# Performance work log

Measured on AMD Instinct MI355X. Metric: run time of the kernel, lower is better.

Reference implementation:

```python
import jax, jax.numpy as jnp
import numpy as np

C = 256      # MSA_channels
PC = 256     # pair_channels
G = 4        # groups
GP = C // G  # group_planes
FF = 4 * C
EPS = 1e-5


def layernorm(x, w, b):
    mu = jnp.mean(x, axis=-1, keepdims=True)
    var = jnp.mean(jnp.square(x - mu), axis=-1, keepdims=True)
    return (x - mu) * jax.lax.rsqrt(var + EPS) * w + b


def setup_inputs() -> dict:
    key = jax.random.key(0)
    ks = jax.random.split(key, 12)
    N, D, L = 1, 64, 512
    s = lambda fan_in: 1.0 / np.sqrt(fan_in)
    return {
        "msa_matrix": jax.random.normal(ks[0], (N, D, L, C), jnp.float32),
        "rr_edge": jax.random.normal(ks[1], (N, L, L, PC), jnp.float32),
        "ln_msa_w": jnp.ones((C,), jnp.float32),
        "ln_msa_b": jnp.zeros((C,), jnp.float32),
        "ln_rr_w": jnp.ones((PC,), jnp.float32),
        "ln_rr_b": jnp.zeros((PC,), jnp.float32),
        "WA": jax.random.normal(ks[2], (PC, G), jnp.float32) * s(PC),
        "bA": jnp.zeros((G,), jnp.float32),
        "WV": jax.random.normal(ks[3], (C, C), jnp.float32) * s(C),
        "bV": jnp.zeros((C,), jnp.float32),
        "WO": jax.random.normal(ks[4], (C, C), jnp.float32) * s(C),
        "bO": jnp.zeros((C,), jnp.float32),
        "ln_ff_w": jnp.ones((C,), jnp.float32),
        "ln_ff_b": jnp.zeros((C,), jnp.float32),
        "W1": jax.random.normal(ks[5], (C, FF), jnp.float32) * s(C),
        "b1": jnp.zeros((FF,), jnp.float32),
        "W2": jax.random.normal(ks[6], (FF, C), jnp.float32) * s(FF),
        "b2": jnp.zeros((C,), jnp.float32),
    }


def reference(msa_matrix, rr_edge, ln_msa_w, ln_msa_b, ln_rr_w, ln_rr_b,
              WA, bA, WV, bV, WO, bO, ln_ff_w, ln_ff_b, W1, b1, W2, b2):
    N, D, L, _ = msa_matrix.shape
    raw = msa_matrix
    m = layernorm(msa_matrix, ln_msa_w, ln_msa_b)          # [N,D,L,C]
    E = 0.5 * (rr_edge + jnp.swapaxes(rr_edge, 1, 2))      # symmetrize [N,L,L,PC]
    E = layernorm(E, ln_rr_w, ln_rr_b)
    A = jax.nn.softmax(E @ WA + bA, axis=2)                # [N,L,L,G], softmax over key dim j
    V = (m @ WV + bV).reshape(N, D, L, G, GP)              # [N,D,L,G,GP]
    agg = jnp.einsum('nijg,ndjgc->ndigc', A, V).reshape(N, D, L, C)
    out = agg @ WO + bO
    x = raw + out                                          # residual (dropout = identity at eval)
    h = layernorm(x, ln_ff_w, ln_ff_b)                     # FFN with pre-LN + residual
    return x + (jax.nn.relu(h @ W1 + b1) @ W2 + b2)
```

## Files before the change

### kernel.cpp

```cpp
#include <hip/hip_runtime.h>
#include <hip/hip_bf16.h>

typedef __bf16 bf16;
typedef bf16 bf16x8 __attribute__((ext_vector_type(8)));
typedef bf16 bf16x4v __attribute__((ext_vector_type(4)));
typedef float f32x4 __attribute__((ext_vector_type(4)));

#define LN_EPS 1e-5f

__global__ __launch_bounds__(256) void ln_rows_kernel(
    const float* __restrict__ in, const float* __restrict__ w,
    const float* __restrict__ b, bf16* __restrict__ out)
{
  int row = blockIdx.x * 4 + (threadIdx.x >> 6);
  int lane = threadIdx.x & 63;
  const float4* p = (const float4*)(in + (size_t)row * 256);
  float4 v = p[lane];
  float s = v.x + v.y + v.z + v.w;
  float q = v.x*v.x + v.y*v.y + v.z*v.z + v.w*v.w;
  #pragma unroll
  for (int o = 32; o; o >>= 1) { s += __shfl_xor(s, o); q += __shfl_xor(q, o); }
  float mu = s * (1.0f/256.0f);
  float rs = rsqrtf(q*(1.0f/256.0f) - mu*mu + LN_EPS);
  float4 wv = ((const float4*)w)[lane];
  float4 bv = ((const float4*)b)[lane];
  bf16x4v o4;
  o4[0] = (bf16)((v.x - mu)*rs*wv.x + bv.x);
  o4[1] = (bf16)((v.y - mu)*rs*wv.y + bv.y);
  o4[2] = (bf16)((v.z - mu)*rs*wv.z + bv.z);
  o4[3] = (bf16)((v.w - mu)*rs*wv.w + bv.w);
  *(bf16x4v*)(out + (size_t)row * 256 + lane * 4) = o4;
}

__global__ __launch_bounds__(256) void transpose_f32_bf16(
    const float* __restrict__ in, bf16* __restrict__ out, int R, int C)
{
  __shared__ float tile[32][33];
  int bc = blockIdx.x * 32, br = blockIdx.y * 32;
  int tx = threadIdx.x, ty = threadIdx.y;
  #pragma unroll
  for (int i = ty; i < 32; i += 8)
    tile[i][tx] = in[(size_t)(br + i) * C + bc + tx];
  __syncthreads();
  #pragma unroll
  for (int i = ty; i < 32; i += 8)
    out[(size_t)(bc + i) * R + br + tx] = (bf16)tile[tx][i];
}

__global__ __launch_bounds__(256) void sym_ln_wa_kernel(
    const float* __restrict__ rr, const float* __restrict__ w,
    const float* __restrict__ b, const float* __restrict__ WA,
    float* __restrict__ S)
{
  int rem = blockIdx.x; int ti = 0; int len = 32;
  while (rem >= len) { rem -= len; ti++; len--; }
  int tj = ti + rem;
  int wid = threadIdx.x >> 6, lane = threadIdx.x & 63;
  int c0 = lane * 4;
  float4 wv = ((const float4*)w)[lane];
  float4 bv = ((const float4*)b)[lane];
  const float4* wa4 = (const float4*)WA;
  float4 wa0 = wa4[c0+0], wa1 = wa4[c0+1], wa2 = wa4[c0+2], wa3 = wa4[c0+3];
  int pend = blockIdx.y * 128 + 128;
  for (int p = blockIdx.y * 128 + wid; p < pend; p += 4) {
    int i = ti*16 + (p >> 4), j = tj*16 + (p & 15);
    float4 a = ((const float4*)(rr + ((size_t)i*512 + j)*256))[lane];
    float4 c = ((const float4*)(rr + ((size_t)j*512 + i)*256))[lane];
    float ex = 0.5f*(a.x + c.x), ey = 0.5f*(a.y + c.y),
          ez = 0.5f*(a.z + c.z), ew = 0.5f*(a.w + c.w);
    float s = ex+ey+ez+ew;
    float q = ex*ex+ey*ey+ez*ez+ew*ew;
    #pragma unroll
    for (int o = 32; o; o >>= 1) { s += __shfl_xor(s, o); q += __shfl_xor(q, o); }
    float mu = s*(1.f/256.f);
    float rs = rsqrtf(q*(1.f/256.f) - mu*mu + LN_EPS);
    float nx = (ex-mu)*rs*wv.x + bv.x;
    float ny = (ey-mu)*rs*wv.y + bv.y;
    float nz = (ez-mu)*rs*wv.z + bv.z;
    float nw = (ew-mu)*rs*wv.w + bv.w;
    float g0 = nx*wa0.x + ny*wa1.x + nz*wa2.x + nw*wa3.x;
    float g1 = nx*wa0.y + ny*wa1.y + nz*wa2.y + nw*wa3.y;
    float g2 = nx*wa0.z + ny*wa1.z + nz*wa2.z + nw*wa3.z;
    float g3 = nx*wa0.w + ny*wa1.w + nz*wa2.w + nw*wa3.w;
    #pragma unroll
    for (int o = 32; o; o >>= 1) {
      g0 += __shfl_xor(g0, o); g1 += __shfl_xor(g1, o);
      g2 += __shfl_xor(g2, o); g3 += __shfl_xor(g3, o);
    }
    if (lane == 0) {
      float4 r4 = make_float4(g0, g1, g2, g3);
      ((float4*)S)[(size_t)i*512 + j] = r4;
      ((float4*)S)[(size_t)j*512 + i] = r4;
    }
  }
}

__global__ __launch_bounds__(256) void softmax_kernel(
    const float* __restrict__ S, bf16* __restrict__ Aout)
{
  int i = blockIdx.x * 4 + (threadIdx.x >> 6);
  int lane = threadIdx.x & 63;
  const float4* Sr = (const float4*)S + (size_t)i * 512;
  float4 s[8];
  float m0 = -1e30f, m1 = -1e30f, m2 = -1e30f, m3 = -1e30f;
  #pragma unroll
  for (int it = 0; it < 8; it++) {
    s[it] = Sr[lane + it*64];
    m0 = fmaxf(m0, s[it].x); m1 = fmaxf(m1, s[it].y);
    m2 = fmaxf(m2, s[it].z); m3 = fmaxf(m3, s[it].w);
  }
  #pragma unroll
  for (int o = 32; o; o >>= 1) {
    m0 = fmaxf(m0, __shfl_xor(m0, o)); m1 = fmaxf(m1, __shfl_xor(m1, o));
    m2 = fmaxf(m2, __shfl_xor(m2, o)); m3 = fmaxf(m3, __shfl_xor(m3, o));
  }
  float t0=0.f, t1=0.f, t2=0.f, t3=0.f;
  #pragma unroll
  for (int it = 0; it < 8; it++) {
    s[it].x = __expf(s[it].x - m0); t0 += s[it].x;
    s[it].y = __expf(s[it].y - m1); t1 += s[it].y;
    s[it].z = __expf(s[it].z - m2); t2 += s[it].z;
    s[it].w = __expf(s[it].w - m3); t3 += s[it].w;
  }
  #pragma unroll
  for (int o = 32; o; o >>= 1) {
    t0 += __shfl_xor(t0, o); t1 += __shfl_xor(t1, o);
    t2 += __shfl_xor(t2, o); t3 += __shfl_xor(t3, o);
  }
  t0 = 1.f/t0; t1 = 1.f/t1; t2 = 1.f/t2; t3 = 1.f/t3;
  bf16* A0 = Aout + (size_t)i * 512;
  #pragma unroll
  for (int it = 0; it < 8; it++) {
    int j = lane + it*64;
    A0[j]          = (bf16)(s[it].x * t0);
    A0[262144 + j] = (bf16)(s[it].y * t1);
    A0[524288 + j] = (bf16)(s[it].z * t2);
    A0[786432 + j] = (bf16)(s[it].w * t3);
  }
}

template<int MODE>
__global__ __launch_bounds__(256) void gemm_bt_kernel(
    const bf16* __restrict__ Aglob, const bf16* __restrict__ Bglob,
    void* __restrict__ outP, const float* __restrict__ bias,
    const float* __restrict__ resid, int M, int N, int K)
{
  __shared__ bf16 As[128][40];
  __shared__ bf16 Bs[128][40];
  int g = blockIdx.z;
  const bf16* Ag = Aglob;
  const bf16* Bg = Bglob;
  if (MODE == 1) { Ag += (size_t)g * 512 * 512; Bg += (size_t)g * 4096 * 512; }
  int bm = blockIdx.y * 128, bn = blockIdx.x * 128;
  int tid = threadIdx.x;
  int wid = tid >> 6, lane = tid & 63;
  int wm = (wid >> 1) * 64, wn = (wid & 1) * 64;
  f32x4 acc[4][4];
  #pragma unroll
  for (int mi = 0; mi < 4; mi++)
    #pragma unroll
    for (int ni = 0; ni < 4; ni++)
      acc[mi][ni] = (f32x4){0.f, 0.f, 0.f, 0.f};
  int r0 = tid >> 2;
  int koff = (tid & 3) * 8;
  int fr = lane & 15, fk = (lane >> 4) * 8;
  for (int k0 = 0; k0 < K; k0 += 32) {
    __syncthreads();
    *(bf16x8*)&As[r0][koff]    = *(const bf16x8*)&Ag[(size_t)(bm + r0) * K + k0 + koff];
    *(bf16x8*)&As[r0+64][koff] = *(const bf16x8*)&Ag[(size_t)(bm + r0 + 64) * K + k0 + koff];
    *(bf16x8*)&Bs[r0][koff]    = *(const bf16x8*)&Bg[(size_t)(bn + r0) * K + k0 + koff];
    *(bf16x8*)&Bs[r0+64][koff] = *(const bf16x8*)&Bg[(size_t)(bn + r0 + 64) * K + k0 + koff];
    __syncthreads();
    bf16x8 af[4], bf_[4];
    #pragma unroll
    for (int mi = 0; mi < 4; mi++) af[mi] = *(const bf16x8*)&As[wm + mi*16 + fr][fk];
    #pragma unroll
    for (int ni = 0; ni < 4; ni++) bf_[ni] = *(const bf16x8*)&Bs[wn + ni*16 + fr][fk];
    #pragma unroll
    for (int mi = 0; mi < 4; mi++)
      #pragma unroll
      for (int ni = 0; ni < 4; ni++)
        acc[mi][ni] = __builtin_amdgcn_mfma_f32_16x16x32_bf16(af[mi], bf_[ni], acc[mi][ni], 0, 0, 0);
  }
  int cn0 = lane & 15;
  int rq = (lane >> 4) * 4;
  #pragma unroll
  for (int mi = 0; mi < 4; mi++) {
    #pragma unroll
    for (int ni = 0; ni < 4; ni++) {
      int mb = bm + wm + mi*16 + rq;
      int nc = bn + wn + ni*16 + cn0;
      #pragma unroll
      for (int r = 0; r < 4; r++) {
        int mr = mb + r;
        float v = acc[mi][ni][r];
        if (MODE == 0) {
          v += bias[mr];
          int gg = mr >> 6, rp = mr & 63, d = nc >> 9, j = nc & 511;
          ((bf16*)outP)[((size_t)gg*4096 + d*64 + rp)*512 + j] = (bf16)v;
        } else if (MODE == 1) {
          int d = nc >> 6, c6 = nc & 63;
          ((bf16*)outP)[((size_t)d*512 + mr)*256 + g*64 + c6] = (bf16)v;
        } else if (MODE == 2) {
          v += bias[nc] + resid[(size_t)mr * N + nc];
          ((float*)outP)[(size_t)mr * N + nc] = v;
        } else {
          v = fmaxf(v + bias[nc], 0.f);
          ((bf16*)outP)[(size_t)mr * N + nc] = (bf16)v;
        }
      }
    }
  }
}

extern "C" void kernel_launch(void* const* d_in, const int* in_sizes, int n_in,
                              void* d_out, int out_size, void* d_ws, size_t ws_size,
                              hipStream_t stream)
{
  (void)in_sizes; (void)n_in; (void)out_size; (void)ws_size;
  const float* msa = (const float*)d_in[0];
  const float* rr  = (const float*)d_in[1];
  const float* lmw = (const float*)d_in[2];
  const float* lmb = (const float*)d_in[3];
  const float* lrw = (const float*)d_in[4];
  const float* lrb = (const float*)d_in[5];
  const float* WA  = (const float*)d_in[6];
  const float* WV  = (const float*)d_in[8];
  const float* bV  = (const float*)d_in[9];
  const float* WO  = (const float*)d_in[10];
  const float* bO  = (const float*)d_in[11];
  const float* lfw = (const float*)d_in[12];
  const float* lfb = (const float*)d_in[13];
  const float* W1  = (const float*)d_in[14];
  const float* b1  = (const float*)d_in[15];
  const float* W2  = (const float*)d_in[16];
  const float* b2  = (const float*)d_in[17];
  float* out = (float*)d_out;
  char* ws = (char*)d_ws;
  bf16* tbuf = (bf16*)(ws + 0);
  float* S   = (float*)(ws + 0);
  bf16* Abuf = (bf16*)(ws + 4194304);
  bf16* m    = (bf16*)(ws + 6291456);
  bf16* Vt   = (bf16*)(ws + 23068672);
  bf16* agg  = (bf16*)(ws + 39845888);
  bf16* h    = (bf16*)(ws + 67108864);
  bf16* WVt  = (bf16*)(ws + 83886080);
  bf16* WOt  = WVt + 65536;
  bf16* W1t  = WOt + 65536;
  bf16* W2t  = W1t + 262144;

  dim3 tb(32, 8);
  transpose_f32_bf16<<<dim3(8, 8),  tb, 0, stream>>>(WV, WVt, 256, 256);
  transpose_f32_bf16<<<dim3(8, 8),  tb, 0, stream>>>(WO, WOt, 256, 256);
  transpose_f32_bf16<<<dim3(32, 8), tb, 0, stream>>>(W1, W1t, 256, 1024);
  transpose_f32_bf16<<<dim3(8, 32), tb, 0, stream>>>(W2, W2t, 1024, 256);

  ln_rows_kernel<<<8192, 256, 0, stream>>>(msa, lmw, lmb, m);
  sym_ln_wa_kernel<<<dim3(528, 2), 256, 0, stream>>>(rr, lrw, lrb, WA, S);
  gemm_bt_kernel<0><<<dim3(256, 2, 1), 256, 0, stream>>>(WVt, m, Vt, bV, nullptr, 256, 32768, 256);
  softmax_kernel<<<128, 256, 0, stream>>>(S, Abuf);
  gemm_bt_kernel<1><<<dim3(32, 4, 4), 256, 0, stream>>>(Abuf, Vt, agg, nullptr, nullptr, 512, 4096, 512);
  gemm_bt_kernel<2><<<dim3(2, 256, 1), 256, 0, stream>>>(agg, WOt, out, bO, msa, 32768, 256, 256);
  ln_rows_kernel<<<8192, 256, 0, stream>>>(out, lfw, lfb, h);
  gemm_bt_kernel<3><<<dim3(8, 256, 1), 256, 0, stream>>>(h, W1t, tbuf, b1, nullptr, 32768, 1024, 256);
  gemm_bt_kernel<2><<<dim3(2, 256, 1), 256, 0, stream>>>(tbuf, W2t, out, b2, out, 32768, 256, 1024);
}
```

Baseline: 258.1 us.

## Use direct global-to-LDS loads in GEMM, merge transposes, split sym-LN grid

The GEMM tile loads now use the global_load_lds builtin, which writes 16 bytes per lane straight into unpadded shared memory and skips the register round trip. Each wave loads two 16-row chunks laid out row-major. The four weight transposes are merged into a single launch, and the symmetrize-LN kernel's grid is doubled in y so each block handles half as many pairs. Dropping the padding may add LDS bank conflicts on the fragment reads, and the direct-to-LDS path has stricter alignment and layout requirements.

```diff
diff --git a/kernel.cpp b/kernel.cpp
--- a/kernel.cpp
+++ b/kernel.cpp
@@ -7,6 +7,12 @@
 typedef float f32x4 __attribute__((ext_vector_type(4)));
 
 #define LN_EPS 1e-5f
+
+__device__ __forceinline__ void gload_lds16(const bf16* gsrc, bf16* ldst) {
+  __builtin_amdgcn_global_load_lds(
+      (const __attribute__((address_space(1))) void*)gsrc,
+      (__attribute__((address_space(3))) void*)ldst, 16, 0, 0);
+}
 
 __global__ __launch_bounds__(256) void ln_rows_kernel(
     const float* __restrict__ in, const float* __restrict__ w,
@@ -32,11 +38,20 @@
   *(bf16x4v*)(out + (size_t)row * 256 + lane * 4) = o4;
 }
 
-__global__ __launch_bounds__(256) void transpose_f32_bf16(
-    const float* __restrict__ in, bf16* __restrict__ out, int R, int C)
+__global__ __launch_bounds__(256) void transpose_all_kernel(
+    const float* __restrict__ WV, const float* __restrict__ WO,
+    const float* __restrict__ W1, const float* __restrict__ W2,
+    bf16* __restrict__ WVt, bf16* __restrict__ WOt,
+    bf16* __restrict__ W1t, bf16* __restrict__ W2t)
 {
   __shared__ float tile[32][33];
-  int bc = blockIdx.x * 32, br = blockIdx.y * 32;
+  int id = blockIdx.x;
+  const float* in; bf16* out; int R, C, tpr;
+  if (id < 64)       { in = WV; out = WVt; R = 256;  C = 256;  tpr = 8;  }
+  else if (id < 128) { in = WO; out = WOt; R = 256;  C = 256;  tpr = 8;  id -= 64; }
+  else if (id < 384) { in = W1; out = W1t; R = 256;  C = 1024; tpr = 32; id -= 128; }
+  else               { in = W2; out = W2t; R = 1024; C = 256;  tpr = 8;  id -= 384; }
+  int bc = (id % tpr) * 32, br = (id / tpr) * 32;
   int tx = threadIdx.x, ty = threadIdx.y;
   #pragma unroll
   for (int i = ty; i < 32; i += 8)
@@ -61,8 +76,8 @@
   float4 bv = ((const float4*)b)[lane];
   const float4* wa4 = (const float4*)WA;
   float4 wa0 = wa4[c0+0], wa1 = wa4[c0+1], wa2 = wa4[c0+2], wa3 = wa4[c0+3];
-  int pend = blockIdx.y * 128 + 128;
-  for (int p = blockIdx.y * 128 + wid; p < pend; p += 4) {
+  int pend = blockIdx.y * 64 + 64;
+  for (int p = blockIdx.y * 64 + wid; p < pend; p += 4) {
     int i = ti*16 + (p >> 4), j = tj*16 + (p & 15);
     float4 a = ((const float4*)(rr + ((size_t)i*512 + j)*256))[lane];
     float4 c = ((const float4*)(rr + ((size_t)j*512 + i)*256))[lane];
@@ -145,8 +160,8 @@
     void* __restrict__ outP, const float* __restrict__ bias,
     const float* __restrict__ resid, int M, int N, int K)
 {
-  __shared__ bf16 As[128][40];
-  __shared__ bf16 Bs[128][40];
+  __shared__ bf16 As[128 * 32];
+  __shared__ bf16 Bs[128 * 32];
   int g = blockIdx.z;
   const bf16* Ag = Aglob;
   const bf16* Bg = Bglob;
@@ -161,21 +176,26 @@
     #pragma unroll
     for (int ni = 0; ni < 4; ni++)
       acc[mi][ni] = (f32x4){0.f, 0.f, 0.f, 0.f};
-  int r0 = tid >> 2;
-  int koff = (tid & 3) * 8;
+  int c0 = wid * 2, c1 = wid * 2 + 1;
+  int srow = lane >> 2;
+  int scol = (lane & 3) * 8;
+  const bf16* a0 = &Ag[(size_t)(bm + c0*16 + srow) * K + scol];
+  const bf16* a1 = &Ag[(size_t)(bm + c1*16 + srow) * K + scol];
+  const bf16* b0 = &Bg[(size_t)(bn + c0*16 + srow) * K + scol];
+  const bf16* b1 = &Bg[(size_t)(bn + c1*16 + srow) * K + scol];
   int fr = lane & 15, fk = (lane >> 4) * 8;
   for (int k0 = 0; k0 < K; k0 += 32) {
     __syncthreads();
-    *(bf16x8*)&As[r0][koff]    = *(const bf16x8*)&Ag[(size_t)(bm + r0) * K + k0 + koff];
-    *(bf16x8*)&As[r0+64][koff] = *(const bf16x8*)&Ag[(size_t)(bm + r0 + 64) * K + k0 + koff];
-    *(bf16x8*)&Bs[r0][koff]    = *(const bf16x8*)&Bg[(size_t)(bn + r0) * K + k0 + koff];
-    *(bf16x8*)&Bs[r0+64][koff] = *(const bf16x8*)&Bg[(size_t)(bn + r0 + 64) * K + k0 + koff];
+    gload_lds16(a0 + k0, &As[c0 * 512]);
+    gload_lds16(a1 + k0, &As[c1 * 512]);
+    gload_lds16(b0 + k0, &Bs[c0 * 512]);
+    gload_lds16(b1 + k0, &Bs[c1 * 512]);
     __syncthreads();
     bf16x8 af[4], bf_[4];
     #pragma unroll
-    for (int mi = 0; mi < 4; mi++) af[mi] = *(const bf16x8*)&As[wm + mi*16 + fr][fk];
-    #pragma unroll
-    for (int ni = 0; ni < 4; ni++) bf_[ni] = *(const bf16x8*)&Bs[wn + ni*16 + fr][fk];
+    for (int mi = 0; mi < 4; mi++) af[mi] = *(const bf16x8*)&As[(wm + mi*16 + fr) * 32 + fk];
+    #pragma unroll
+    for (int ni = 0; ni < 4; ni++) bf_[ni] = *(const bf16x8*)&Bs[(wn + ni*16 + fr) * 32 + fk];
     #pragma unroll
     for (int mi = 0; mi < 4; mi++)
       #pragma unroll
@@ -249,14 +269,10 @@
   bf16* W1t  = WOt + 65536;
   bf16* W2t  = W1t + 262144;
 
-  dim3 tb(32, 8);
-  transpose_f32_bf16<<<dim3(8, 8),  tb, 0, stream>>>(WV, WVt, 256, 256);
-  transpose_f32_bf16<<<dim3(8, 8),  tb, 0, stream>>>(WO, WOt, 256, 256);
-  transpose_f32_bf16<<<dim3(32, 8), tb, 0, stream>>>(W1, W1t, 256, 1024);
-  transpose_f32_bf16<<<dim3(8, 32), tb, 0, stream>>>(W2, W2t, 1024, 256);
+  transpose_all_kernel<<<640, dim3(32, 8), 0, stream>>>(WV, WO, W1, W2, WVt, WOt, W1t, W2t);
 
   ln_rows_kernel<<<8192, 256, 0, stream>>>(msa, lmw, lmb, m);
-  sym_ln_wa_kernel<<<dim3(528, 2), 256, 0, stream>>>(rr, lrw, lrb, WA, S);
+  sym_ln_wa_kernel<<<dim3(528, 4), 256, 0, stream>>>(rr, lrw, lrb, WA, S);
   gemm_bt_kernel<0><<<dim3(256, 2, 1), 256, 0, stream>>>(WVt, m, Vt, bV, nullptr, 256, 32768, 256);
   softmax_kernel<<<128, 256, 0, stream>>>(S, Abuf);
   gemm_bt_kernel<1><<<dim3(32, 4, 4), 256, 0, stream>>>(Abuf, Vt, agg, nullptr, nullptr, 512, 4096, 512);
```

After: 249.6 us. 1.03x faster.
